# Kernel optimization log

Hardware: AMD Instinct MI355X
Metric: run time of the kernel (lower is better)

Reference implementation:

```python
import jax, jax.numpy as jnp
import numpy as np

VOCAB, X_SIZE, H_SIZE, N_CLASSES = 50000, 300, 150, 5
DEPTH = 18                      # complete binary tree, N = 2^(DEPTH+1)-1 nodes
N_NODES = 2 ** (DEPTH + 1) - 1  # 524287
SCALE = 0.05                    # param init scale for numerical sanity


def setup_inputs() -> dict:
    key = jax.random.key(0)
    ks = jax.random.split(key, 8)
    return {
        "x_id": jax.random.randint(ks[0], (N_NODES,), 0, VOCAB, dtype=jnp.int32),
        "emb": jax.random.normal(ks[1], (VOCAB, X_SIZE), jnp.float32) * SCALE,
        "W_iou": jax.random.normal(ks[2], (X_SIZE, 3 * H_SIZE), jnp.float32) * SCALE,
        "U_iou": jax.random.normal(ks[3], (H_SIZE, 3 * H_SIZE), jnp.float32) * SCALE,
        "b_iou": jnp.zeros((3 * H_SIZE,), jnp.float32),
        "W_f": jax.random.normal(ks[4], (X_SIZE, H_SIZE), jnp.float32) * SCALE,
        "U_f": jax.random.normal(ks[5], (H_SIZE, H_SIZE), jnp.float32) * SCALE,
        "b_f": jnp.zeros((H_SIZE,), jnp.float32),
        "W_out": jax.random.normal(ks[6], (H_SIZE, N_CLASSES), jnp.float32) * SCALE,
        "b_out": jnp.zeros((N_CLASSES,), jnp.float32),
    }


def reference(x_id, emb, W_iou, U_iou, b_iou, W_f, U_f, b_f, W_out, b_out):
    # Child-Sum TreeLSTM propagated leaves->root over a complete binary tree
    # stored in heap layout: children of node i are 2i+1, 2i+2.
    N = x_id.shape[0]
    H = U_iou.shape[0]
    depth = int(np.log2(N + 1)) - 1

    x = emb[x_id]  # input_module: embedding lookup  [N, X]
    h = jnp.zeros((N, H), x.dtype)
    c = jnp.zeros((N, H), x.dtype)

    # level-batched topological propagation (19 static levels)
    for lvl in range(depth, -1, -1):
        s, e = 2 ** lvl - 1, 2 ** (lvl + 1) - 1  # node range of this level
        xl = x[s:e]                              # [n_l, X]
        if lvl == depth:  # leaves: zero child state
            h_sum = jnp.zeros((e - s, H), x.dtype)
            fc_sum = jnp.zeros((e - s, H), x.dtype)
        else:
            # children of consecutive nodes are contiguous: [2s+1, 2e+1)
            hc = h[2 * s + 1:2 * e + 1].reshape(e - s, 2, H)
            cc = c[2 * s + 1:2 * e + 1].reshape(e - s, 2, H)
            h_sum = hc.sum(axis=1)               # reduce: sum child h
            # per-child forget gate
            f = jax.nn.sigmoid((xl @ W_f)[:, None, :] + hc @ U_f + b_f)
            fc_sum = (f * cc).sum(axis=1)
        iou = xl @ W_iou + h_sum @ U_iou + b_iou  # [n_l, 3H]
        i, o, u = jnp.split(iou, 3, axis=-1)
        c_new = jax.nn.sigmoid(i) * jnp.tanh(u) + fc_sum
        h_new = jax.nn.sigmoid(o) * jnp.tanh(c_new)
        h = h.at[s:e].set(h_new)
        c = c.at[s:e].set(c_new)

    return h @ W_out + b_out  # output_module: Linear(H, C)  [N, C]
```

## Files before the change

kernel.cpp:

```cpp
#include <hip/hip_runtime.h>
#include <cstdint>

typedef _Float16 f16_t;
typedef __attribute__((ext_vector_type(8))) _Float16 f16x8;
typedef __attribute__((ext_vector_type(4))) _Float16 f16x4;
typedef __attribute__((ext_vector_type(4))) float f32x4;

#define HP      160
#define NCOL    640
#define KXP     320
#define NNODES  524287
#define LEAF_S  262143
#define LEAF_M  262144
#define NVOCAB  50000
#define AST     168

__device__ __forceinline__ float frcp(float x) { return __builtin_amdgcn_rcpf(x); }
__device__ __forceinline__ float sigf(float x) { return frcp(1.0f + __expf(-x)); }
__device__ __forceinline__ float tanhf_(float x) {
  return 1.0f - 2.0f * frcp(1.0f + __expf(2.0f * x));
}
__device__ __forceinline__ f16x8 zero8() {
  f16x8 z;
#pragma unroll
  for (int i = 0; i < 8; ++i) z[i] = (_Float16)0.0f;
  return z;
}
__device__ __forceinline__ f32x4 zero4() {
  f32x4 z;
#pragma unroll
  for (int i = 0; i < 4; ++i) z[i] = 0.0f;
  return z;
}

__global__ void prep_params(const float* __restrict__ W_iou, const float* __restrict__ U_iou,
                            const float* __restrict__ b_iou, const float* __restrict__ W_f,
                            const float* __restrict__ U_f, const float* __restrict__ b_f,
                            f16_t* __restrict__ WreT, f16_t* __restrict__ UreT,
                            float* __restrict__ bre) {
  int idx = blockIdx.x * 256 + threadIdx.x;
  if (idx < NCOL * KXP) {
    int col = idx / KXP, k = idx % KXP;
    int j = col >> 2, g = col & 3;
    float v = 0.0f;
    if (k < 300 && j < 150) v = (g < 3) ? W_iou[k * 450 + g * 150 + j] : W_f[k * 150 + j];
    WreT[idx] = (f16_t)v;
  } else if (idx < NCOL * KXP + NCOL * HP) {
    int i2 = idx - NCOL * KXP;
    int col = i2 / HP, k = i2 % HP;
    int g = col / 160, j = col % 160;
    float v = 0.0f;
    if (k < 150 && j < 150) v = (g < 3) ? U_iou[k * 450 + g * 150 + j] : U_f[k * 150 + j];
    UreT[i2] = (f16_t)v;
  } else if (idx < NCOL * KXP + NCOL * HP + NCOL) {
    int col = idx - (NCOL * KXP + NCOL * HP);
    int j = col >> 2, g = col & 3;
    bre[col] = (j < 150) ? ((g < 3) ? b_iou[g * 150 + j] : b_f[j]) : 0.0f;
  }
}

__global__ __launch_bounds__(256) void gemm_p(const float* __restrict__ emb,
                                              const f16_t* __restrict__ WreT,
                                              const float* __restrict__ bre,
                                              f16_t* __restrict__ P) {
  __shared__ __align__(16) f16_t A_sh[64 * 328];
  __shared__ __align__(16) f16_t B_sh[128 * 40];
  const int tid = threadIdx.x;
  const int wid = tid >> 6, lane = tid & 63, l15 = lane & 15, q = lane >> 4;
  const int row0 = blockIdx.x * 64;

#pragma unroll
  for (int i = 0; i < 10; ++i) {
    int ch = tid + 256 * i;
    int r = ch / 40, kc = (ch % 40) * 8;
    int grow = row0 + r;
    f16x8 hv;
    if (grow < NVOCAB && kc + 8 <= 300) {
      float4 a = *(const float4*)&emb[grow * 300 + kc];
      float4 b = *(const float4*)&emb[grow * 300 + kc + 4];
      hv[0] = (_Float16)a.x; hv[1] = (_Float16)a.y; hv[2] = (_Float16)a.z; hv[3] = (_Float16)a.w;
      hv[4] = (_Float16)b.x; hv[5] = (_Float16)b.y; hv[6] = (_Float16)b.z; hv[7] = (_Float16)b.w;
    } else {
#pragma unroll
      for (int e = 0; e < 8; ++e) {
        int k = kc + e;
        float v = (grow < NVOCAB && k < 300) ? emb[grow * 300 + k] : 0.0f;
        hv[e] = (_Float16)v;
      }
    }
    *(f16x8*)&A_sh[r * 328 + kc] = hv;
  }
  __syncthreads();

  for (int bn = 0; bn < 5; ++bn) {
    const int col0 = bn * 128;
    f32x4 acc[8];
#pragma unroll
    for (int t = 0; t < 8; ++t) acc[t] = zero4();
    for (int kk = 0; kk < KXP; kk += 32) {
#pragma unroll
      for (int i = 0; i < 2; ++i) {
        int ch = tid + 256 * i;
        int cidx = ch >> 2, kc = (ch & 3) * 8;
        *(f16x8*)&B_sh[cidx * 40 + kc] =
            *(const f16x8*)&WreT[(col0 + cidx) * KXP + kk + kc];
      }
      __syncthreads();
      f16x8 af = *(const f16x8*)&A_sh[(16 * wid + l15) * 328 + kk + q * 8];
#pragma unroll
      for (int t = 0; t < 8; ++t) {
        f16x8 bfr = *(const f16x8*)&B_sh[(t * 16 + l15) * 40 + q * 8];
        acc[t] = __builtin_amdgcn_mfma_f32_16x16x32_f16(af, bfr, acc[t], 0, 0, 0);
      }
      __syncthreads();
    }
#pragma unroll
    for (int t = 0; t < 8; ++t) {
      int col = col0 + t * 16 + l15;
      float bias = bre[col];
#pragma unroll
      for (int r2 = 0; r2 < 4; ++r2) {
        int row = row0 + 16 * wid + q * 4 + r2;
        if (row < NVOCAB) P[(long)row * NCOL + col] = (f16_t)(acc[t][r2] + bias);
      }
    }
  }
}

__global__ void leafhc_kernel(const f16_t* __restrict__ P, f16_t* __restrict__ Hleaf,
                              f16_t* __restrict__ Cleaf) {
  int idx = blockIdx.x * 256 + threadIdx.x;
  if (idx >= NVOCAB * 80) return;
  int v = idx / 80, t = idx % 80;
  f16x8 pk = *(const f16x8*)&P[(long)v * NCOL + t * 8];
#pragma unroll
  for (int e = 0; e < 2; ++e) {
    float iv = (float)pk[e * 4 + 0], ov = (float)pk[e * 4 + 1], uv = (float)pk[e * 4 + 2];
    float cl = sigf(iv) * tanhf_(uv);
    float hl = sigf(ov) * tanhf_(cl);
    Hleaf[(long)v * HP + t * 2 + e] = (f16_t)hl;
    Cleaf[(long)v * HP + t * 2 + e] = (f16_t)cl;
  }
}

__global__ void oleaf_kernel(const f16_t* __restrict__ Hleaf, const float* __restrict__ W_out,
                             const float* __restrict__ b_out, float* __restrict__ Oleaf) {
  const int tid = threadIdx.x;
  const int row = blockIdx.x * 16 + (tid >> 4), l = tid & 15;
  if (row >= NVOCAB) return;
  float acc[5] = {0, 0, 0, 0, 0};
  for (int j = l; j < 150; j += 16) {
    float hv = (float)Hleaf[(long)row * HP + j];
#pragma unroll
    for (int m = 0; m < 5; ++m) acc[m] += hv * W_out[j * 5 + m];
  }
#pragma unroll
  for (int m = 0; m < 5; ++m) {
    float vv = acc[m];
    vv += __shfl_xor(vv, 1);
    vv += __shfl_xor(vv, 2);
    vv += __shfl_xor(vv, 4);
    vv += __shfl_xor(vv, 8);
    if (l == 0) Oleaf[(long)row * 8 + m] = vv + b_out[m];
  }
}

__global__ void leafout_kernel(const int* __restrict__ x_id, const float* __restrict__ Oleaf,
                               float* __restrict__ out) {
  int leaf = blockIdx.x * 256 + threadIdx.x;
  int xv = x_id[LEAF_S + leaf];
  const float* O = Oleaf + (long)xv * 8;
  float4 o4 = *(const float4*)O;
  float o5 = O[4];
  long base = ((long)LEAF_S + leaf) * 5;
  out[base + 0] = o4.x; out[base + 1] = o4.y; out[base + 2] = o4.z;
  out[base + 3] = o4.w; out[base + 4] = o5;
}

template <bool LEAF>
__global__ __launch_bounds__(256, 3) void fused_kernel(
    const int* __restrict__ x_id, const f16_t* __restrict__ P,
    const f16_t* __restrict__ UreT, const f16_t* __restrict__ Hc,
    const f16_t* __restrict__ Cc, f16_t* __restrict__ Hout,
    f16_t* __restrict__ Cout, const float* __restrict__ W_out,
    const float* __restrict__ b_out, float* __restrict__ out, int s1, int M1) {
  __shared__ __align__(16) f16_t A_sh[64 * AST];
  __shared__ __align__(16) f16_t A2_sh[32 * AST];
  __shared__ __align__(16) f16_t B_sh[128 * 40];
  __shared__ f16_t C_sh[32 * 160];
  const int tid = threadIdx.x;
  const int wid = tid >> 6, lane = tid & 63, l15 = lane & 15, q = lane >> 4;
  const int p0 = blockIdx.x * 32;
  const long childbase = 2L * s1 + 1 + 2 * p0;

#pragma unroll
  for (int i = 0; i < 5; ++i) {
    int ch = tid + 256 * i;
    int r = ch / 20, kc = (ch % 20) * 8;
    f16x8 v;
    if (LEAF) {
      int xv = x_id[childbase + r];
      v = *(const f16x8*)&Hc[(long)xv * HP + kc];
    } else {
      v = *(const f16x8*)&Hc[(long)(2 * p0 + r) * HP + kc];
    }
    *(f16x8*)&A_sh[r * AST + kc] = v;
  }
  __syncthreads();

  int xvp[2], xvl[2], xvr[2];
#pragma unroll
  for (int rr = 0; rr < 2; ++rr) {
    int pl = 8 * wid + 2 * q + rr;
    long pn = (long)s1 + p0 + pl;
    xvp[rr] = x_id[pn];
    if (LEAF) {
      xvl[rr] = x_id[childbase + 2 * pl];
      xvr[rr] = x_id[childbase + 2 * pl + 1];
    }
  }
  float oacc1[2][5] = {};

  for (int jt = 0; jt < 5; ++jt) {
    const int j0 = jt * 32;
    f32x4 acc[4][2];
#pragma unroll
    for (int g = 0; g < 4; ++g)
#pragma unroll
      for (int jh = 0; jh < 2; ++jh) acc[g][jh] = zero4();

    for (int kk = 0; kk < HP; kk += 32) {
#pragma unroll
      for (int i = 0; i < 2; ++i) {
        int ch = tid + 256 * i;
        int cidx = ch >> 2, kc = (ch & 3) * 8;
        int g = cidx >> 5, jj = cidx & 31;
        int col = g * HP + j0 + jj;
        *(f16x8*)&B_sh[cidx * 40 + kc] = *(const f16x8*)&UreT[col * HP + kk + kc];
      }
      __syncthreads();
      f16x8 af = *(const f16x8*)&A_sh[(16 * wid + l15) * AST + kk + q * 8];
#pragma unroll
      for (int g = 0; g < 4; ++g)
#pragma unroll
        for (int jh = 0; jh < 2; ++jh) {
          f16x8 bfr = *(const f16x8*)&B_sh[(g * 32 + jh * 16 + l15) * 40 + q * 8];
          acc[g][jh] = __builtin_amdgcn_mfma_f32_16x16x32_f16(af, bfr, acc[g][jh], 0, 0, 0);
        }
      __syncthreads();
    }

#pragma unroll
    for (int rr = 0; rr < 2; ++rr) {
      const int r = rr * 2;
      const int lr0 = 16 * wid + q * 4 + r;
      const int pl = lr0 >> 1;
      const f16_t* Prp = P + (long)xvp[rr] * NCOL;
#pragma unroll
      for (int jh = 0; jh < 2; ++jh) {
        const int j = j0 + jh * 16 + l15;
        f16x4 pp = *(const f16x4*)&Prp[j * 4];
        float ipre = (float)pp[0] + acc[0][jh][r] + acc[0][jh][r + 1];
        float opre = (float)pp[1] + acc[1][jh][r] + acc[1][jh][r + 1];
        float upre = (float)pp[2] + acc[2][jh][r] + acc[2][jh][r + 1];
        float pf   = (float)pp[3];
        float fl = sigf(pf + acc[3][jh][r]);
        float fr = sigf(pf + acc[3][jh][r + 1]);
        float clv, crv;
        if (LEAF) {
          clv = (float)Cc[(long)xvl[rr] * HP + j];
          crv = (float)Cc[(long)xvr[rr] * HP + j];
        } else {
          clv = (float)Cc[(long)(2 * p0 + lr0) * HP + j];
          crv = (float)Cc[(long)(2 * p0 + lr0 + 1) * HP + j];
        }
        float cn = sigf(ipre) * tanhf_(upre) + fl * clv + fr * crv;
        float hn = sigf(opre) * tanhf_(cn);
        A2_sh[pl * AST + j] = (f16_t)hn;
        C_sh[pl * 160 + j] = (f16_t)cn;
        int wbase = (j < 150) ? j * 5 : 0;
#pragma unroll
        for (int m = 0; m < 5; ++m) oacc1[rr][m] += hn * W_out[wbase + m];
      }
    }
  }

#pragma unroll
  for (int rr = 0; rr < 2; ++rr) {
    int pl = 8 * wid + 2 * q + rr;
#pragma unroll
    for (int m = 0; m < 5; ++m) {
      float v = oacc1[rr][m];
      v += __shfl_xor(v, 1);
      v += __shfl_xor(v, 2);
      v += __shfl_xor(v, 4);
      v += __shfl_xor(v, 8);
      if (l15 == 0) out[((long)s1 + p0 + pl) * 5 + m] = v + b_out[m];
    }
  }

  const int s2 = (s1 - 1) >> 1;
  const int p02 = p0 >> 1;
  const bool act2 = (wid < 2);
  int xvp2[2];
#pragma unroll
  for (int rr = 0; rr < 2; ++rr) {
    int pl = 8 * wid + 2 * q + rr;
    long pn = (long)s2 + p02 + (act2 ? pl : 0);
    xvp2[rr] = x_id[pn];
  }
  float oacc2[2][5] = {};

  for (int jt = 0; jt < 5; ++jt) {
    const int j0 = jt * 32;
    f32x4 acc[4][2];
#pragma unroll
    for (int g = 0; g < 4; ++g)
#pragma unroll
      for (int jh = 0; jh < 2; ++jh) acc[g][jh] = zero4();

    for (int kk = 0; kk < HP; kk += 32) {
#pragma unroll
      for (int i = 0; i < 2; ++i) {
        int ch = tid + 256 * i;
        int cidx = ch >> 2, kc = (ch & 3) * 8;
        int g = cidx >> 5, jj = cidx & 31;
        int col = g * HP + j0 + jj;
        *(f16x8*)&B_sh[cidx * 40 + kc] = *(const f16x8*)&UreT[col * HP + kk + kc];
      }
      __syncthreads();
      if (act2) {
        f16x8 af = *(const f16x8*)&A2_sh[(16 * wid + l15) * AST + kk + q * 8];
#pragma unroll
        for (int g = 0; g < 4; ++g)
#pragma unroll
          for (int jh = 0; jh < 2; ++jh) {
            f16x8 bfr = *(const f16x8*)&B_sh[(g * 32 + jh * 16 + l15) * 40 + q * 8];
            acc[g][jh] = __builtin_amdgcn_mfma_f32_16x16x32_f16(af, bfr, acc[g][jh], 0, 0, 0);
          }
      }
      __syncthreads();
    }

    if (act2) {
#pragma unroll
      for (int rr = 0; rr < 2; ++rr) {
        const int r = rr * 2;
        const int lr0 = 16 * wid + q * 4 + r;
        const int pl = lr0 >> 1;
        const f16_t* Prp = P + (long)xvp2[rr] * NCOL;
#pragma unroll
        for (int jh = 0; jh < 2; ++jh) {
          const int j = j0 + jh * 16 + l15;
          f16x4 pp = *(const f16x4*)&Prp[j * 4];
          float ipre = (float)pp[0] + acc[0][jh][r] + acc[0][jh][r + 1];
          float opre = (float)pp[1] + acc[1][jh][r] + acc[1][jh][r + 1];
          float upre = (float)pp[2] + acc[2][jh][r] + acc[2][jh][r + 1];
          float pf   = (float)pp[3];
          float fl = sigf(pf + acc[3][jh][r]);
          float fr = sigf(pf + acc[3][jh][r + 1]);
          float clv = (float)C_sh[lr0 * 160 + j];
          float crv = (float)C_sh[(lr0 + 1) * 160 + j];
          float cn = sigf(ipre) * tanhf_(upre) + fl * clv + fr * crv;
          float hn = sigf(opre) * tanhf_(cn);
          Hout[(long)(p02 + pl) * HP + j] = (f16_t)hn;
          Cout[(long)(p02 + pl) * HP + j] = (f16_t)cn;
          int wbase = (j < 150) ? j * 5 : 0;
#pragma unroll
          for (int m = 0; m < 5; ++m) oacc2[rr][m] += hn * W_out[wbase + m];
        }
      }
    }
  }

  if (act2) {
#pragma unroll
    for (int rr = 0; rr < 2; ++rr) {
      int pl = 8 * wid + 2 * q + rr;
#pragma unroll
      for (int m = 0; m < 5; ++m) {
        float v = oacc2[rr][m];
        v += __shfl_xor(v, 1);
        v += __shfl_xor(v, 2);
        v += __shfl_xor(v, 4);
        v += __shfl_xor(v, 8);
        if (l15 == 0) out[((long)s2 + p02 + pl) * 5 + m] = v + b_out[m];
      }
    }
  }
}

__device__ __forceinline__ void level_tile(
    const int* __restrict__ x_id, const f16_t* __restrict__ P,
    const f16_t* __restrict__ UreT, const f16_t* __restrict__ h_child,
    const f16_t* __restrict__ c_child, f16_t* __restrict__ h_par,
    f16_t* __restrict__ c_par, const float* Wo, const float* __restrict__ b_out,
    float* __restrict__ out, int s, int M, int p0, f16_t* A_sh, f16_t* B_sh) {
  const int tid = threadIdx.x;
  const int wid = tid >> 6, lane = tid & 63, l15 = lane & 15, q = lane >> 4;
  int rowsValid = 2 * M - 2 * p0;
  if (rowsValid > 64) rowsValid = 64;

#pragma unroll
  for (int i = 0; i < 5; ++i) {
    int ch = tid + 256 * i;
    int r = ch / 20, kc = (ch % 20) * 8;
    f16x8 v;
    if (r < rowsValid) v = *(const f16x8*)&h_child[(long)(2 * p0 + r) * HP + kc];
    else v = zero8();
    *(f16x8*)&A_sh[r * 184 + kc] = v;
  }
  __syncthreads();

  int xvp[2]; long pnode[2]; int plg[2]; bool valid[2]; int lr0v[2];
#pragma unroll
  for (int rr = 0; rr < 2; ++rr) {
    int lr0 = 16 * wid + q * 4 + rr * 2;
    int pl = lr0 >> 1;
    valid[rr] = (p0 + pl) < M;
    long pn = (long)s + p0 + (valid[rr] ? pl : 0);
    pnode[rr] = pn; plg[rr] = p0 + pl; lr0v[rr] = lr0;
    xvp[rr] = x_id[pn];
  }

  float oacc[2][5];
#pragma unroll
  for (int rr = 0; rr < 2; ++rr)
#pragma unroll
    for (int m = 0; m < 5; ++m) oacc[rr][m] = 0.0f;

  for (int jt = 0; jt < 5; ++jt) {
    const int j0 = jt * 32;
    f32x4 acc[4][2];
#pragma unroll
    for (int g = 0; g < 4; ++g)
#pragma unroll
      for (int jh = 0; jh < 2; ++jh) acc[g][jh] = zero4();

    for (int kk = 0; kk < HP; kk += 32) {
#pragma unroll
      for (int i = 0; i < 2; ++i) {
        int ch = tid + 256 * i;
        int cidx = ch >> 2, kc = (ch & 3) * 8;
        int g = cidx >> 5, jj = cidx & 31;
        int col = g * HP + j0 + jj;
        *(f16x8*)&B_sh[cidx * 40 + kc] = *(const f16x8*)&UreT[col * HP + kk + kc];
      }
      __syncthreads();
      f16x8 af = *(const f16x8*)&A_sh[(16 * wid + l15) * 184 + kk + q * 8];
#pragma unroll
      for (int g = 0; g < 4; ++g)
#pragma unroll
        for (int jh = 0; jh < 2; ++jh) {
          f16x8 bfr = *(const f16x8*)&B_sh[(g * 32 + jh * 16 + l15) * 40 + q * 8];
          acc[g][jh] = __builtin_amdgcn_mfma_f32_16x16x32_f16(af, bfr, acc[g][jh], 0, 0, 0);
        }
      __syncthreads();
    }

#pragma unroll
    for (int rr = 0; rr < 2; ++rr) {
      const int r = rr * 2;
      const f16_t* Prp = P + (long)xvp[rr] * NCOL;
#pragma unroll
      for (int jh = 0; jh < 2; ++jh) {
        const int j = j0 + jh * 16 + l15;
        f16x4 pp = *(const f16x4*)&Prp[j * 4];
        float ipre = (float)pp[0] + acc[0][jh][r] + acc[0][jh][r + 1];
        float opre = (float)pp[1] + acc[1][jh][r] + acc[1][jh][r + 1];
        float upre = (float)pp[2] + acc[2][jh][r] + acc[2][jh][r + 1];
        float pf   = (float)pp[3];
        float fl = sigf(pf + acc[3][jh][r]);
        float fr = sigf(pf + acc[3][jh][r + 1]);
        float clv = valid[rr] ? (float)c_child[(long)(2 * p0 + lr0v[rr]) * HP + j] : 0.0f;
        float crv = valid[rr] ? (float)c_child[(long)(2 * p0 + lr0v[rr] + 1) * HP + j] : 0.0f;
        float cn = sigf(ipre) * tanhf_(upre) + fl * clv + fr * crv;
        float hn = sigf(opre) * tanhf_(cn);
        if (valid[rr]) {
          h_par[(long)plg[rr] * HP + j] = (f16_t)hn;
          c_par[(long)plg[rr] * HP + j] = (f16_t)cn;
        }
#pragma unroll
        for (int m = 0; m < 5; ++m) oacc[rr][m] += hn * Wo[j * 5 + m];
      }
    }
  }

#pragma unroll
  for (int rr = 0; rr < 2; ++rr) {
#pragma unroll
    for (int m = 0; m < 5; ++m) {
      float v = oacc[rr][m];
      v += __shfl_xor(v, 1);
      v += __shfl_xor(v, 2);
      v += __shfl_xor(v, 4);
      v += __shfl_xor(v, 8);
      if (l15 == 0 && valid[rr]) out[pnode[rr] * 5 + m] = v + b_out[m];
    }
  }
}

__global__ __launch_bounds__(256, 4) void tail_kernel(
    const int* __restrict__ x_id, const f16_t* __restrict__ P,
    const f16_t* __restrict__ UreT, f16_t* __restrict__ HA, f16_t* __restrict__ HB,
    f16_t* __restrict__ CA, f16_t* __restrict__ CB, const float* __restrict__ W_out,
    const float* __restrict__ b_out, float* __restrict__ out) {
  __shared__ __align__(16) f16_t A_sh[64 * 184];
  __shared__ __align__(16) f16_t B_sh[128 * 40];
  __shared__ float Wo[800];
  for (int i = threadIdx.x; i < 800; i += 256) Wo[i] = (i < 750) ? W_out[i] : 0.0f;
  for (int lvl = 5; lvl >= 0; --lvl) {
    int s = (1 << lvl) - 1, M = 1 << lvl;
    const f16_t* hc = ((lvl + 1) & 1) ? HA : HB;
    const f16_t* cc = ((lvl + 1) & 1) ? CA : CB;
    f16_t* hp = (lvl & 1) ? HA : HB;
    f16_t* cp = (lvl & 1) ? CA : CB;
    level_tile(x_id, P, UreT, hc, cc, hp, cp, Wo, b_out, out, s, M, 0, A_sh, B_sh);
    __syncthreads();
  }
}

extern "C" void kernel_launch(void* const* d_in, const int* in_sizes, int n_in,
                              void* d_out, int out_size, void* d_ws, size_t ws_size,
                              hipStream_t stream) {
  const int* x_id   = (const int*)d_in[0];
  const float* emb  = (const float*)d_in[1];
  const float* W_iou = (const float*)d_in[2];
  const float* U_iou = (const float*)d_in[3];
  const float* b_iou = (const float*)d_in[4];
  const float* W_f   = (const float*)d_in[5];
  const float* U_f   = (const float*)d_in[6];
  const float* b_f   = (const float*)d_in[7];
  const float* W_out = (const float*)d_in[8];
  const float* b_out = (const float*)d_in[9];
  float* out = (float*)d_out;
  char* ws = (char*)d_ws;

  f16_t* WreT  = (f16_t*)(ws + 0);
  f16_t* UreT  = (f16_t*)(ws + 409600);
  float* bre   = (float*)(ws + 614400);
  f16_t* P     = (f16_t*)(ws + 616960);
  f16_t* Hleaf = (f16_t*)(ws + 64616960);
  f16_t* Cleaf = (f16_t*)(ws + 80616960);
  float* Oleaf = (float*)(ws + 96616960);
  f16_t* HX    = (f16_t*)(ws + 98216960);
  f16_t* HY    = (f16_t*)(ws + 119188480);
  f16_t* CX    = (f16_t*)(ws + 140160000);
  f16_t* CY    = (f16_t*)(ws + 161131520);

  prep_params<<<1203, 256, 0, stream>>>(W_iou, U_iou, b_iou, W_f, U_f, b_f, WreT, UreT, bre);
  gemm_p<<<782, 256, 0, stream>>>(emb, WreT, bre, P);
  leafhc_kernel<<<15625, 256, 0, stream>>>(P, Hleaf, Cleaf);
  oleaf_kernel<<<3125, 256, 0, stream>>>(Hleaf, W_out, b_out, Oleaf);
  leafout_kernel<<<1024, 256, 0, stream>>>(x_id, Oleaf, out);

  fused_kernel<true><<<4096, 256, 0, stream>>>(x_id, P, UreT, Hleaf, Cleaf, HX, CX,
                                               W_out, b_out, out, (1 << 17) - 1, 1 << 17);
  fused_kernel<false><<<1024, 256, 0, stream>>>(x_id, P, UreT, HX, CX, HY, CY,
                                                W_out, b_out, out, (1 << 15) - 1, 1 << 15);
  fused_kernel<false><<<256, 256, 0, stream>>>(x_id, P, UreT, HY, CY, HX, CX,
                                               W_out, b_out, out, (1 << 13) - 1, 1 << 13);
  fused_kernel<false><<<64, 256, 0, stream>>>(x_id, P, UreT, HX, CX, HY, CY,
                                              W_out, b_out, out, (1 << 11) - 1, 1 << 11);
  fused_kernel<false><<<16, 256, 0, stream>>>(x_id, P, UreT, HY, CY, HX, CX,
                                              W_out, b_out, out, (1 << 9) - 1, 1 << 9);
  fused_kernel<false><<<4, 256, 0, stream>>>(x_id, P, UreT, HX, CX, HY, CY,
                                             W_out, b_out, out, (1 << 7) - 1, 1 << 7);
  tail_kernel<<<1, 256, 0, stream>>>(x_id, P, UreT, HX, HY, CX, CY, W_out, b_out, out);

  (void)in_sizes; (void)n_in; (void)out_size; (void)ws_size;
}
```

Before: 866.5 us.

## Restructure level kernels: per-level launches, fused child output projection, padded LDS

Removes the separate leaf output kernels and instead computes the output projection for each level's child rows inside the kernel that loads them into shared memory, using staged W_out tiles. The two-level fused kernels for upper levels are replaced by single-level level_k launches (levels 15..6), while the leaf-adjacent level keeps a fused two-level kernel. B and C shared tiles get new strides (36, 162) with split 4-wide accesses, presumably to reduce LDS bank conflicts. The change trades fewer inter-level fusions and more launches for removing gather-heavy leaf output passes and per-thread output accumulation in the epilogues.

```diff
diff --git a/kernel.cpp b/kernel.cpp
--- a/kernel.cpp
+++ b/kernel.cpp
@@ -11,9 +11,10 @@
 #define KXP     320
 #define NNODES  524287
 #define LEAF_S  262143
-#define LEAF_M  262144
 #define NVOCAB  50000
 #define AST     168
+#define BST     36
+#define CST     162
 
 __device__ __forceinline__ float frcp(float x) { return __builtin_amdgcn_rcpf(x); }
 __device__ __forceinline__ float sigf(float x) { return frcp(1.0f + __expf(-x)); }
@@ -31,6 +32,28 @@
 #pragma unroll
   for (int i = 0; i < 4; ++i) z[i] = 0.0f;
   return z;
+}
+
+__device__ __forceinline__ void stage_B(const f16_t* __restrict__ UreT, f16_t* B_sh,
+                                        int tid, int j0, int kk) {
+#pragma unroll
+  for (int i = 0; i < 2; ++i) {
+    int ch = tid + 256 * i;
+    int cidx = ch >> 2, kc = (ch & 3) * 8;
+    int g = cidx >> 5, jj = cidx & 31;
+    int col = g * HP + j0 + jj;
+    f16x8 v = *(const f16x8*)&UreT[col * HP + kk + kc];
+    f16x4 lo = {v[0], v[1], v[2], v[3]};
+    f16x4 hi = {v[4], v[5], v[6], v[7]};
+    *(f16x4*)&B_sh[cidx * BST + kc] = lo;
+    *(f16x4*)&B_sh[cidx * BST + kc + 4] = hi;
+  }
+}
+__device__ __forceinline__ f16x8 read_B(const f16_t* B_sh, int tile16, int q) {
+  f16x4 lo = *(const f16x4*)&B_sh[tile16 * BST + q * 8];
+  f16x4 hi = *(const f16x4*)&B_sh[tile16 * BST + q * 8 + 4];
+  f16x8 v = {lo[0], lo[1], lo[2], lo[3], hi[0], hi[1], hi[2], hi[3]};
+  return v;
 }
 
 __global__ void prep_params(const float* __restrict__ W_iou, const float* __restrict__ U_iou,
@@ -143,70 +166,65 @@
   }
 }
 
-__global__ void oleaf_kernel(const f16_t* __restrict__ Hleaf, const float* __restrict__ W_out,
-                             const float* __restrict__ b_out, float* __restrict__ Oleaf) {
-  const int tid = threadIdx.x;
-  const int row = blockIdx.x * 16 + (tid >> 4), l = tid & 15;
-  if (row >= NVOCAB) return;
-  float acc[5] = {0, 0, 0, 0, 0};
-  for (int j = l; j < 150; j += 16) {
-    float hv = (float)Hleaf[(long)row * HP + j];
-#pragma unroll
-    for (int m = 0; m < 5; ++m) acc[m] += hv * W_out[j * 5 + m];
-  }
-#pragma unroll
-  for (int m = 0; m < 5; ++m) {
-    float vv = acc[m];
-    vv += __shfl_xor(vv, 1);
-    vv += __shfl_xor(vv, 2);
-    vv += __shfl_xor(vv, 4);
-    vv += __shfl_xor(vv, 8);
-    if (l == 0) Oleaf[(long)row * 8 + m] = vv + b_out[m];
-  }
-}
-
-__global__ void leafout_kernel(const int* __restrict__ x_id, const float* __restrict__ Oleaf,
-                               float* __restrict__ out) {
-  int leaf = blockIdx.x * 256 + threadIdx.x;
-  int xv = x_id[LEAF_S + leaf];
-  const float* O = Oleaf + (long)xv * 8;
-  float4 o4 = *(const float4*)O;
-  float o5 = O[4];
-  long base = ((long)LEAF_S + leaf) * 5;
-  out[base + 0] = o4.x; out[base + 1] = o4.y; out[base + 2] = o4.z;
-  out[base + 3] = o4.w; out[base + 4] = o5;
-}
-
-template <bool LEAF>
-__global__ __launch_bounds__(256, 3) void fused_kernel(
+__global__ __launch_bounds__(256, 3) void fused17_kernel(
     const int* __restrict__ x_id, const f16_t* __restrict__ P,
-    const f16_t* __restrict__ UreT, const f16_t* __restrict__ Hc,
-    const f16_t* __restrict__ Cc, f16_t* __restrict__ Hout,
+    const f16_t* __restrict__ UreT, const f16_t* __restrict__ Hleaf,
+    const f16_t* __restrict__ Cleaf, f16_t* __restrict__ Hout,
     f16_t* __restrict__ Cout, const float* __restrict__ W_out,
-    const float* __restrict__ b_out, float* __restrict__ out, int s1, int M1) {
+    const float* __restrict__ b_out, float* __restrict__ out) {
   __shared__ __align__(16) f16_t A_sh[64 * AST];
   __shared__ __align__(16) f16_t A2_sh[32 * AST];
-  __shared__ __align__(16) f16_t B_sh[128 * 40];
-  __shared__ f16_t C_sh[32 * 160];
+  __shared__ __align__(16) f16_t B_sh[128 * BST];
+  __shared__ f16_t C_sh[32 * CST];
+  __shared__ __align__(16) f16_t Wo16[160 * 8];
   const int tid = threadIdx.x;
   const int wid = tid >> 6, lane = tid & 63, l15 = lane & 15, q = lane >> 4;
   const int p0 = blockIdx.x * 32;
-  const long childbase = 2L * s1 + 1 + 2 * p0;
+  const int s1 = (1 << 17) - 1;
+  const long childbase = (long)LEAF_S + 2 * p0;
+
+  for (int idx = tid; idx < 1280; idx += 256) {
+    int j = idx >> 3, m = idx & 7;
+    Wo16[idx] = (j < 150 && m < 5) ? (f16_t)W_out[j * 5 + m] : (f16_t)0.0f;
+  }
 
 #pragma unroll
   for (int i = 0; i < 5; ++i) {
     int ch = tid + 256 * i;
     int r = ch / 20, kc = (ch % 20) * 8;
-    f16x8 v;
-    if (LEAF) {
-      int xv = x_id[childbase + r];
-      v = *(const f16x8*)&Hc[(long)xv * HP + kc];
-    } else {
-      v = *(const f16x8*)&Hc[(long)(2 * p0 + r) * HP + kc];
-    }
-    *(f16x8*)&A_sh[r * AST + kc] = v;
+    int xv = x_id[childbase + r];
+    *(f16x8*)&A_sh[r * AST + kc] = *(const f16x8*)&Hleaf[(long)xv * HP + kc];
   }
   __syncthreads();
+
+  {
+    const int row = 16 * wid + l15;
+    const int jb = q * 40;
+    float o[5] = {0, 0, 0, 0, 0};
+#pragma unroll
+    for (int jc = 0; jc < 5; ++jc) {
+      f16x8 hv8 = *(const f16x8*)&A_sh[row * AST + jb + jc * 8];
+#pragma unroll
+      for (int e = 0; e < 8; ++e) {
+        float hv = (float)hv8[e];
+        f16x8 w8 = *(const f16x8*)&Wo16[(jb + jc * 8 + e) * 8];
+#pragma unroll
+        for (int m = 0; m < 5; ++m) o[m] += hv * (float)w8[m];
+      }
+    }
+#pragma unroll
+    for (int m = 0; m < 5; ++m) {
+      float v = o[m];
+      v += __shfl_xor(v, 16);
+      v += __shfl_xor(v, 32);
+      o[m] = v;
+    }
+    if (q == 0) {
+      long base = (childbase + row) * 5;
+#pragma unroll
+      for (int m = 0; m < 5; ++m) out[base + m] = o[m] + b_out[m];
+    }
+  }
 
   int xvp[2], xvl[2], xvr[2];
 #pragma unroll
@@ -214,12 +232,9 @@
     int pl = 8 * wid + 2 * q + rr;
     long pn = (long)s1 + p0 + pl;
     xvp[rr] = x_id[pn];
-    if (LEAF) {
-      xvl[rr] = x_id[childbase + 2 * pl];
-      xvr[rr] = x_id[childbase + 2 * pl + 1];
-    }
-  }
-  float oacc1[2][5] = {};
+    xvl[rr] = x_id[childbase + 2 * pl];
+    xvr[rr] = x_id[childbase + 2 * pl + 1];
+  }
 
   for (int jt = 0; jt < 5; ++jt) {
     const int j0 = jt * 32;
@@ -230,21 +245,14 @@
       for (int jh = 0; jh < 2; ++jh) acc[g][jh] = zero4();
 
     for (int kk = 0; kk < HP; kk += 32) {
-#pragma unroll
-      for (int i = 0; i < 2; ++i) {
-        int ch = tid + 256 * i;
-        int cidx = ch >> 2, kc = (ch & 3) * 8;
-        int g = cidx >> 5, jj = cidx & 31;
-        int col = g * HP + j0 + jj;
-        *(f16x8*)&B_sh[cidx * 40 + kc] = *(const f16x8*)&UreT[col * HP + kk + kc];
-      }
+      stage_B(UreT, B_sh, tid, j0, kk);
       __syncthreads();
       f16x8 af = *(const f16x8*)&A_sh[(16 * wid + l15) * AST + kk + q * 8];
 #pragma unroll
       for (int g = 0; g < 4; ++g)
 #pragma unroll
         for (int jh = 0; jh < 2; ++jh) {
-          f16x8 bfr = *(const f16x8*)&B_sh[(g * 32 + jh * 16 + l15) * 40 + q * 8];
+          f16x8 bfr = read_B(B_sh, g * 32 + jh * 16 + l15, q);
           acc[g][jh] = __builtin_amdgcn_mfma_f32_16x16x32_f16(af, bfr, acc[g][jh], 0, 0, 0);
         }
       __syncthreads();
@@ -253,9 +261,10 @@
 #pragma unroll
     for (int rr = 0; rr < 2; ++rr) {
       const int r = rr * 2;
-      const int lr0 = 16 * wid + q * 4 + r;
-      const int pl = lr0 >> 1;
+      const int pl = 8 * wid + 2 * q + rr;
       const f16_t* Prp = P + (long)xvp[rr] * NCOL;
+      const f16_t* Prl = Cleaf + (long)xvl[rr] * HP;
+      const f16_t* Prr_ = Cleaf + (long)xvr[rr] * HP;
 #pragma unroll
       for (int jh = 0; jh < 2; ++jh) {
         const int j = j0 + jh * 16 + l15;
@@ -266,36 +275,43 @@
         float pf   = (float)pp[3];
         float fl = sigf(pf + acc[3][jh][r]);
         float fr = sigf(pf + acc[3][jh][r + 1]);
-        float clv, crv;
-        if (LEAF) {
-          clv = (float)Cc[(long)xvl[rr] * HP + j];
-          crv = (float)Cc[(long)xvr[rr] * HP + j];
-        } else {
-          clv = (float)Cc[(long)(2 * p0 + lr0) * HP + j];
-          crv = (float)Cc[(long)(2 * p0 + lr0 + 1) * HP + j];
-        }
+        float clv = (float)Prl[j];
+        float crv = (float)Prr_[j];
         float cn = sigf(ipre) * tanhf_(upre) + fl * clv + fr * crv;
         float hn = sigf(opre) * tanhf_(cn);
         A2_sh[pl * AST + j] = (f16_t)hn;
-        C_sh[pl * 160 + j] = (f16_t)cn;
-        int wbase = (j < 150) ? j * 5 : 0;
-#pragma unroll
-        for (int m = 0; m < 5; ++m) oacc1[rr][m] += hn * W_out[wbase + m];
-      }
-    }
-  }
-
-#pragma unroll
-  for (int rr = 0; rr < 2; ++rr) {
-    int pl = 8 * wid + 2 * q + rr;
+        C_sh[pl * CST + j] = (f16_t)cn;
+      }
+    }
+  }
+  __syncthreads();
+
+  if (wid < 2) {
+    const int row = 16 * wid + l15;
+    const int jb = q * 40;
+    float o[5] = {0, 0, 0, 0, 0};
+#pragma unroll
+    for (int jc = 0; jc < 5; ++jc) {
+      f16x8 hv8 = *(const f16x8*)&A2_sh[row * AST + jb + jc * 8];
+#pragma unroll
+      for (int e = 0; e < 8; ++e) {
+        float hv = (float)hv8[e];
+        f16x8 w8 = *(const f16x8*)&Wo16[(jb + jc * 8 + e) * 8];
+#pragma unroll
+        for (int m = 0; m < 5; ++m) o[m] += hv * (float)w8[m];
+      }
+    }
 #pragma unroll
     for (int m = 0; m < 5; ++m) {
-      float v = oacc1[rr][m];
-      v += __shfl_xor(v, 1);
-      v += __shfl_xor(v, 2);
-      v += __shfl_xor(v, 4);
-      v += __shfl_xor(v, 8);
-      if (l15 == 0) out[((long)s1 + p0 + pl) * 5 + m] = v + b_out[m];
+      float v = o[m];
+      v += __shfl_xor(v, 16);
+      v += __shfl_xor(v, 32);
+      o[m] = v;
+    }
+    if (q == 0) {
+      long base = ((long)s1 + p0 + row) * 5;
+#pragma unroll
+      for (int m = 0; m < 5; ++m) out[base + m] = o[m] + b_out[m];
     }
   }
 
@@ -309,7 +325,6 @@
     long pn = (long)s2 + p02 + (act2 ? pl : 0);
     xvp2[rr] = x_id[pn];
   }
-  float oacc2[2][5] = {};
 
   for (int jt = 0; jt < 5; ++jt) {
     const int j0 = jt * 32;
@@ -320,14 +335,7 @@
       for (int jh = 0; jh < 2; ++jh) acc[g][jh] = zero4();
 
     for (int kk = 0; kk < HP; kk += 32) {
-#pragma unroll
-      for (int i = 0; i < 2; ++i) {
-        int ch = tid + 256 * i;
-        int cidx = ch >> 2, kc = (ch & 3) * 8;
-        int g = cidx >> 5, jj = cidx & 31;
-        int col = g * HP + j0 + jj;
-        *(f16x8*)&B_sh[cidx * 40 + kc] = *(const f16x8*)&UreT[col * HP + kk + kc];
-      }
+      stage_B(UreT, B_sh, tid, j0, kk);
       __syncthreads();
       if (act2) {
         f16x8 af = *(const f16x8*)&A2_sh[(16 * wid + l15) * AST + kk + q * 8];
@@ -335,7 +343,7 @@
         for (int g = 0; g < 4; ++g)
 #pragma unroll
           for (int jh = 0; jh < 2; ++jh) {
-            f16x8 bfr = *(const f16x8*)&B_sh[(g * 32 + jh * 16 + l15) * 40 + q * 8];
+            f16x8 bfr = read_B(B_sh, g * 32 + jh * 16 + l15, q);
             acc[g][jh] = __builtin_amdgcn_mfma_f32_16x16x32_f16(af, bfr, acc[g][jh], 0, 0, 0);
           }
       }
@@ -359,75 +367,82 @@
           float pf   = (float)pp[3];
           float fl = sigf(pf + acc[3][jh][r]);
           float fr = sigf(pf + acc[3][jh][r + 1]);
-          float clv = (float)C_sh[lr0 * 160 + j];
-          float crv = (float)C_sh[(lr0 + 1) * 160 + j];
+          float clv = (float)C_sh[lr0 * CST + j];
+          float crv = (float)C_sh[(lr0 + 1) * CST + j];
           float cn = sigf(ipre) * tanhf_(upre) + fl * clv + fr * crv;
           float hn = sigf(opre) * tanhf_(cn);
           Hout[(long)(p02 + pl) * HP + j] = (f16_t)hn;
           Cout[(long)(p02 + pl) * HP + j] = (f16_t)cn;
-          int wbase = (j < 150) ? j * 5 : 0;
-#pragma unroll
-          for (int m = 0; m < 5; ++m) oacc2[rr][m] += hn * W_out[wbase + m];
         }
       }
     }
   }
-
-  if (act2) {
-#pragma unroll
-    for (int rr = 0; rr < 2; ++rr) {
-      int pl = 8 * wid + 2 * q + rr;
-#pragma unroll
-      for (int m = 0; m < 5; ++m) {
-        float v = oacc2[rr][m];
-        v += __shfl_xor(v, 1);
-        v += __shfl_xor(v, 2);
-        v += __shfl_xor(v, 4);
-        v += __shfl_xor(v, 8);
-        if (l15 == 0) out[((long)s2 + p02 + pl) * 5 + m] = v + b_out[m];
-      }
-    }
-  }
-}
-
-__device__ __forceinline__ void level_tile(
+}
+
+__global__ __launch_bounds__(256, 4) void level_k(
     const int* __restrict__ x_id, const f16_t* __restrict__ P,
-    const f16_t* __restrict__ UreT, const f16_t* __restrict__ h_child,
-    const f16_t* __restrict__ c_child, f16_t* __restrict__ h_par,
-    f16_t* __restrict__ c_par, const float* Wo, const float* __restrict__ b_out,
-    float* __restrict__ out, int s, int M, int p0, f16_t* A_sh, f16_t* B_sh) {
+    const f16_t* __restrict__ UreT, const f16_t* __restrict__ Hc,
+    const f16_t* __restrict__ Cc, f16_t* __restrict__ Hp,
+    f16_t* __restrict__ Cp, const float* __restrict__ W_out,
+    const float* __restrict__ b_out, float* __restrict__ out, int s, int M) {
+  __shared__ __align__(16) f16_t A_sh[64 * AST];
+  __shared__ __align__(16) f16_t B_sh[128 * BST];
+  __shared__ __align__(16) float Wo[160 * 8];
   const int tid = threadIdx.x;
   const int wid = tid >> 6, lane = tid & 63, l15 = lane & 15, q = lane >> 4;
-  int rowsValid = 2 * M - 2 * p0;
-  if (rowsValid > 64) rowsValid = 64;
+  const int p0 = blockIdx.x * 32;
+  const long childbase = 2L * s + 1 + 2 * p0;
+
+  for (int idx = tid; idx < 1280; idx += 256) {
+    int j = idx >> 3, m = idx & 7;
+    Wo[idx] = (j < 150 && m < 5) ? W_out[j * 5 + m] : 0.0f;
+  }
 
 #pragma unroll
   for (int i = 0; i < 5; ++i) {
     int ch = tid + 256 * i;
     int r = ch / 20, kc = (ch % 20) * 8;
-    f16x8 v;
-    if (r < rowsValid) v = *(const f16x8*)&h_child[(long)(2 * p0 + r) * HP + kc];
-    else v = zero8();
-    *(f16x8*)&A_sh[r * 184 + kc] = v;
+    *(f16x8*)&A_sh[r * AST + kc] = *(const f16x8*)&Hc[(long)(2 * p0 + r) * HP + kc];
   }
   __syncthreads();
 
-  int xvp[2]; long pnode[2]; int plg[2]; bool valid[2]; int lr0v[2];
+  {
+    const int row = 16 * wid + l15;
+    const int jb = q * 40;
+    float o[5] = {0, 0, 0, 0, 0};
+#pragma unroll
+    for (int jc = 0; jc < 5; ++jc) {
+      f16x8 hv8 = *(const f16x8*)&A_sh[row * AST + jb + jc * 8];
+#pragma unroll
+      for (int e = 0; e < 8; ++e) {
+        float hv = (float)hv8[e];
+        int j = jb + jc * 8 + e;
+        float4 w4 = *(const float4*)&Wo[j * 8];
+        float w5 = Wo[j * 8 + 4];
+        o[0] += hv * w4.x; o[1] += hv * w4.y; o[2] += hv * w4.z;
+        o[3] += hv * w4.w; o[4] += hv * w5;
+      }
+    }
+#pragma unroll
+    for (int m = 0; m < 5; ++m) {
+      float v = o[m];
+      v += __shfl_xor(v, 16);
+      v += __shfl_xor(v, 32);
+      o[m] = v;
+    }
+    if (q == 0) {
+      long base = (childbase + row) * 5;
+#pragma unroll
+      for (int m = 0; m < 5; ++m) out[base + m] = o[m] + b_out[m];
+    }
+  }
+
+  int xvp[2];
 #pragma unroll
   for (int rr = 0; rr < 2; ++rr) {
-    int lr0 = 16 * wid + q * 4 + rr * 2;
-    int pl = lr0 >> 1;
-    valid[rr] = (p0 + pl) < M;
-    long pn = (long)s + p0 + (valid[rr] ? pl : 0);
-    pnode[rr] = pn; plg[rr] = p0 + pl; lr0v[rr] = lr0;
-    xvp[rr] = x_id[pn];
-  }
-
-  float oacc[2][5];
-#pragma unroll
-  for (int rr = 0; rr < 2; ++rr)
-#pragma unroll
-    for (int m = 0; m < 5; ++m) oacc[rr][m] = 0.0f;
+    int pl = 8 * wid + 2 * q + rr;
+    xvp[rr] = x_id[(long)s + p0 + pl];
+  }
 
   for (int jt = 0; jt < 5; ++jt) {
     const int j0 = jt * 32;
@@ -438,21 +453,14 @@
       for (int jh = 0; jh < 2; ++jh) acc[g][jh] = zero4();
 
     for (int kk = 0; kk < HP; kk += 32) {
-#pragma unroll
-      for (int i = 0; i < 2; ++i) {
-        int ch = tid + 256 * i;
-        int cidx = ch >> 2, kc = (ch & 3) * 8;
-        int g = cidx >> 5, jj = cidx & 31;
-        int col = g * HP + j0 + jj;
-        *(f16x8*)&B_sh[cidx * 40 + kc] = *(const f16x8*)&UreT[col * HP + kk + kc];
-      }
+      stage_B(UreT, B_sh, tid, j0, kk);
       __syncthreads();
-      f16x8 af = *(const f16x8*)&A_sh[(16 * wid + l15) * 184 + kk + q * 8];
+      f16x8 af = *(const f16x8*)&A_sh[(16 * wid + l15) * AST + kk + q * 8];
 #pragma unroll
       for (int g = 0; g < 4; ++g)
 #pragma unroll
         for (int jh = 0; jh < 2; ++jh) {
-          f16x8 bfr = *(const f16x8*)&B_sh[(g * 32 + jh * 16 + l15) * 40 + q * 8];
+          f16x8 bfr = read_B(B_sh, g * 32 + jh * 16 + l15, q);
           acc[g][jh] = __builtin_amdgcn_mfma_f32_16x16x32_f16(af, bfr, acc[g][jh], 0, 0, 0);
         }
       __syncthreads();
@@ -461,6 +469,8 @@
 #pragma unroll
     for (int rr = 0; rr < 2; ++rr) {
       const int r = rr * 2;
+      const int lr0 = 16 * wid + q * 4 + r;
+      const int pl = lr0 >> 1;
       const f16_t* Prp = P + (long)xvp[rr] * NCOL;
 #pragma unroll
       for (int jh = 0; jh < 2; ++jh) {
@@ -472,51 +482,171 @@
         float pf   = (float)pp[3];
         float fl = sigf(pf + acc[3][jh][r]);
         float fr = sigf(pf + acc[3][jh][r + 1]);
-        float clv = valid[rr] ? (float)c_child[(long)(2 * p0 + lr0v[rr]) * HP + j] : 0.0f;
-        float crv = valid[rr] ? (float)c_child[(long)(2 * p0 + lr0v[rr] + 1) * HP + j] : 0.0f;
+        float clv = (float)Cc[(long)(2 * p0 + lr0) * HP + j];
+        float crv = (float)Cc[(long)(2 * p0 + lr0 + 1) * HP + j];
         float cn = sigf(ipre) * tanhf_(upre) + fl * clv + fr * crv;
         float hn = sigf(opre) * tanhf_(cn);
-        if (valid[rr]) {
-          h_par[(long)plg[rr] * HP + j] = (f16_t)hn;
-          c_par[(long)plg[rr] * HP + j] = (f16_t)cn;
+        Hp[(long)(p0 + pl) * HP + j] = (f16_t)hn;
+        Cp[(long)(p0 + pl) * HP + j] = (f16_t)cn;
+      }
+    }
+  }
+}
+
+__global__ __launch_bounds__(256, 4) void tail_kernel(
+    const int* __restrict__ x_id, const f16_t* __restrict__ P,
+    const f16_t* __restrict__ UreT, f16_t* __restrict__ HX, f16_t* __restrict__ HY,
+    f16_t* __restrict__ CX, f16_t* __restrict__ CY, const float* __restrict__ W_out,
+    const float* __restrict__ b_out, float* __restrict__ out) {
+  __shared__ __align__(16) f16_t A_sh[64 * AST];
+  __shared__ __align__(16) f16_t B_sh[128 * BST];
+  __shared__ __align__(16) float Wo[160 * 8];
+  const int tid = threadIdx.x;
+  const int wid = tid >> 6, lane = tid & 63, l15 = lane & 15, q = lane >> 4;
+
+  for (int idx = tid; idx < 1280; idx += 256) {
+    int j = idx >> 3, m = idx & 7;
+    Wo[idx] = (j < 150 && m < 5) ? W_out[j * 5 + m] : 0.0f;
+  }
+
+  for (int lvl = 5; lvl >= 0; --lvl) {
+    const int s = (1 << lvl) - 1, M = 1 << lvl;
+    const f16_t* hc = (lvl & 1) ? HX : HY;
+    const f16_t* cc = (lvl & 1) ? CX : CY;
+    f16_t* hp = (lvl & 1) ? HY : HX;
+    f16_t* cp = (lvl & 1) ? CY : CX;
+    int rowsValid = 2 * M;
+    if (rowsValid > 64) rowsValid = 64;
+
+    __syncthreads();
+#pragma unroll
+    for (int i = 0; i < 5; ++i) {
+      int ch = tid + 256 * i;
+      int r = ch / 20, kc = (ch % 20) * 8;
+      f16x8 v = (r < rowsValid) ? *(const f16x8*)&hc[(long)r * HP + kc] : zero8();
+      *(f16x8*)&A_sh[r * AST + kc] = v;
+    }
+    __syncthreads();
+
+    {
+      const int row = 16 * wid + l15;
+      if (row < rowsValid) {
+        const int jb = q * 40;
+        float o[5] = {0, 0, 0, 0, 0};
+#pragma unroll
+        for (int jc = 0; jc < 5; ++jc) {
+          f16x8 hv8 = *(const f16x8*)&A_sh[row * AST + jb + jc * 8];
+#pragma unroll
+          for (int e = 0; e < 8; ++e) {
+            float hv = (float)hv8[e];
+            int j = jb + jc * 8 + e;
+            float4 w4 = *(const float4*)&Wo[j * 8];
+            float w5 = Wo[j * 8 + 4];
+            o[0] += hv * w4.x; o[1] += hv * w4.y; o[2] += hv * w4.z;
+            o[3] += hv * w4.w; o[4] += hv * w5;
+          }
         }
 #pragma unroll
-        for (int m = 0; m < 5; ++m) oacc[rr][m] += hn * Wo[j * 5 + m];
-      }
-    }
-  }
-
-#pragma unroll
-  for (int rr = 0; rr < 2; ++rr) {
+        for (int m = 0; m < 5; ++m) {
+          float v = o[m];
+          v += __shfl_xor(v, 16);
+          v += __shfl_xor(v, 32);
+          o[m] = v;
+        }
+        if (q == 0) {
+          long base = (long)(2 * s + 1 + row) * 5;
+#pragma unroll
+          for (int m = 0; m < 5; ++m) out[base + m] = o[m] + b_out[m];
+        }
+      }
+    }
+
+    int xvp[2]; bool valid[2];
+#pragma unroll
+    for (int rr = 0; rr < 2; ++rr) {
+      int pl = 8 * wid + 2 * q + rr;
+      valid[rr] = pl < M;
+      xvp[rr] = x_id[(long)s + (valid[rr] ? pl : 0)];
+    }
+
+    for (int jt = 0; jt < 5; ++jt) {
+      const int j0 = jt * 32;
+      f32x4 acc[4][2];
+#pragma unroll
+      for (int g = 0; g < 4; ++g)
+#pragma unroll
+        for (int jh = 0; jh < 2; ++jh) acc[g][jh] = zero4();
+
+      for (int kk = 0; kk < HP; kk += 32) {
+        stage_B(UreT, B_sh, tid, j0, kk);
+        __syncthreads();
+        f16x8 af = *(const f16x8*)&A_sh[(16 * wid + l15) * AST + kk + q * 8];
+#pragma unroll
+        for (int g = 0; g < 4; ++g)
+#pragma unroll
+          for (int jh = 0; jh < 2; ++jh) {
+            f16x8 bfr = read_B(B_sh, g * 32 + jh * 16 + l15, q);
+            acc[g][jh] = __builtin_amdgcn_mfma_f32_16x16x32_f16(af, bfr, acc[g][jh], 0, 0, 0);
+          }
+        __syncthreads();
+      }
+
+#pragma unroll
+      for (int rr = 0; rr < 2; ++rr) {
+        const int r = rr * 2;
+        const int lr0 = 16 * wid + q * 4 + r;
+        const int pl = lr0 >> 1;
+        const f16_t* Prp = P + (long)xvp[rr] * NCOL;
+#pragma unroll
+        for (int jh = 0; jh < 2; ++jh) {
+          const int j = j0 + jh * 16 + l15;
+          f16x4 pp = *(const f16x4*)&Prp[j * 4];
+          float ipre = (float)pp[0] + acc[0][jh][r] + acc[0][jh][r + 1];
+          float opre = (float)pp[1] + acc[1][jh][r] + acc[1][jh][r + 1];
+          float upre = (float)pp[2] + acc[2][jh][r] + acc[2][jh][r + 1];
+          float pf   = (float)pp[3];
+          float fl = sigf(pf + acc[3][jh][r]);
+          float fr = sigf(pf + acc[3][jh][r + 1]);
+          float clv = valid[rr] ? (float)cc[(long)lr0 * HP + j] : 0.0f;
+          float crv = valid[rr] ? (float)cc[(long)(lr0 + 1) * HP + j] : 0.0f;
+          float cn = sigf(ipre) * tanhf_(upre) + fl * clv + fr * crv;
+          float hn = sigf(opre) * tanhf_(cn);
+          if (valid[rr]) {
+            hp[(long)pl * HP + j] = (f16_t)hn;
+            cp[(long)pl * HP + j] = (f16_t)cn;
+          }
+        }
+      }
+    }
+    __threadfence();
+  }
+
+  __threadfence();
+  __syncthreads();
+  if (tid < 64) {
+    float o[5] = {0, 0, 0, 0, 0};
+    for (int j = tid; j < 150; j += 64) {
+      float hv = (float)HX[j];
+      float4 w4 = *(const float4*)&Wo[j * 8];
+      float w5 = Wo[j * 8 + 4];
+      o[0] += hv * w4.x; o[1] += hv * w4.y; o[2] += hv * w4.z;
+      o[3] += hv * w4.w; o[4] += hv * w5;
+    }
 #pragma unroll
     for (int m = 0; m < 5; ++m) {
-      float v = oacc[rr][m];
+      float v = o[m];
       v += __shfl_xor(v, 1);
       v += __shfl_xor(v, 2);
       v += __shfl_xor(v, 4);
       v += __shfl_xor(v, 8);
-      if (l15 == 0 && valid[rr]) out[pnode[rr] * 5 + m] = v + b_out[m];
-    }
-  }
-}
-
-__global__ __launch_bounds__(256, 4) void tail_kernel(
-    const int* __restrict__ x_id, const f16_t* __restrict__ P,
-    const f16_t* __restrict__ UreT, f16_t* __restrict__ HA, f16_t* __restrict__ HB,
-    f16_t* __restrict__ CA, f16_t* __restrict__ CB, const float* __restrict__ W_out,
-    const float* __restrict__ b_out, float* __restrict__ out) {
-  __shared__ __align__(16) f16_t A_sh[64 * 184];
-  __shared__ __align__(16) f16_t B_sh[128 * 40];
-  __shared__ float Wo[800];
-  for (int i = threadIdx.x; i < 800; i += 256) Wo[i] = (i < 750) ? W_out[i] : 0.0f;
-  for (int lvl = 5; lvl >= 0; --lvl) {
-    int s = (1 << lvl) - 1, M = 1 << lvl;
-    const f16_t* hc = ((lvl + 1) & 1) ? HA : HB;
-    const f16_t* cc = ((lvl + 1) & 1) ? CA : CB;
-    f16_t* hp = (lvl & 1) ? HA : HB;
-    f16_t* cp = (lvl & 1) ? CA : CB;
-    level_tile(x_id, P, UreT, hc, cc, hp, cp, Wo, b_out, out, s, M, 0, A_sh, B_sh);
-    __syncthreads();
+      v += __shfl_xor(v, 16);
+      v += __shfl_xor(v, 32);
+      o[m] = v;
+    }
+    if (tid == 0) {
+#pragma unroll
+      for (int m = 0; m < 5; ++m) out[m] = o[m] + b_out[m];
+    }
   }
 }
 
@@ -542,30 +672,28 @@
   f16_t* P     = (f16_t*)(ws + 616960);
   f16_t* Hleaf = (f16_t*)(ws + 64616960);
   f16_t* Cleaf = (f16_t*)(ws + 80616960);
-  float* Oleaf = (float*)(ws + 96616960);
-  f16_t* HX    = (f16_t*)(ws + 98216960);
-  f16_t* HY    = (f16_t*)(ws + 119188480);
-  f16_t* CX    = (f16_t*)(ws + 140160000);
-  f16_t* CY    = (f16_t*)(ws + 161131520);
+  f16_t* HX    = (f16_t*)(ws + 96616960);
+  f16_t* HY    = (f16_t*)(ws + 117588480);
+  f16_t* CX    = (f16_t*)(ws + 138560000);
+  f16_t* CY    = (f16_t*)(ws + 159531520);
 
   prep_params<<<1203, 256, 0, stream>>>(W_iou, U_iou, b_iou, W_f, U_f, b_f, WreT, UreT, bre);
   gemm_p<<<782, 256, 0, stream>>>(emb, WreT, bre, P);
   leafhc_kernel<<<15625, 256, 0, stream>>>(P, Hleaf, Cleaf);
-  oleaf_kernel<<<3125, 256, 0, stream>>>(Hleaf, W_out, b_out, Oleaf);
-  leafout_kernel<<<1024, 256, 0, stream>>>(x_id, Oleaf, out);
-
-  fused_kernel<true><<<4096, 256, 0, stream>>>(x_id, P, UreT, Hleaf, Cleaf, HX, CX,
-                                               W_out, b_out, out, (1 << 17) - 1, 1 << 17);
-  fused_kernel<false><<<1024, 256, 0, stream>>>(x_id, P, UreT, HX, CX, HY, CY,
-                                                W_out, b_out, out, (1 << 15) - 1, 1 << 15);
-  fused_kernel<false><<<256, 256, 0, stream>>>(x_id, P, UreT, HY, CY, HX, CX,
-                                               W_out, b_out, out, (1 << 13) - 1, 1 << 13);
-  fused_kernel<false><<<64, 256, 0, stream>>>(x_id, P, UreT, HX, CX, HY, CY,
-                                              W_out, b_out, out, (1 << 11) - 1, 1 << 11);
-  fused_kernel<false><<<16, 256, 0, stream>>>(x_id, P, UreT, HY, CY, HX, CX,
-                                              W_out, b_out, out, (1 << 9) - 1, 1 << 9);
-  fused_kernel<false><<<4, 256, 0, stream>>>(x_id, P, UreT, HX, CX, HY, CY,
-                                             W_out, b_out, out, (1 << 7) - 1, 1 << 7);
+
+  fused17_kernel<<<4096, 256, 0, stream>>>(x_id, P, UreT, Hleaf, Cleaf, HX, CX,
+                                           W_out, b_out, out);
+
+  for (int L = 15; L >= 6; --L) {
+    int s = (1 << L) - 1, M = 1 << L;
+    const f16_t* hc = (L & 1) ? HX : HY;
+    const f16_t* cc = (L & 1) ? CX : CY;
+    f16_t* hp = (L & 1) ? HY : HX;
+    f16_t* cp = (L & 1) ? CY : CX;
+    level_k<<<M / 32, 256, 0, stream>>>(x_id, P, UreT, hc, cc, hp, cp,
+                                        W_out, b_out, out, s, M);
+  }
+
   tail_kernel<<<1, 256, 0, stream>>>(x_id, P, UreT, HX, HY, CX, CY, W_out, b_out, out);
 
   (void)in_sizes; (void)n_in; (void)out_size; (void)ws_size;
```

Measured after the change: 896.5 us. +3.5%, slower.
